# Performance work log

Measured on AMD Instinct MI355X. Metric: run time of the kernel, lower is better.

Reference implementation:

```python
import jax, jax.numpy as jnp
import numpy as np

PATCH = 9
RAD = PATCH // 2  # 4


def _spatial_correlation(a, b):
    """SpatialCorrelationSampler(kernel_size=1, patch_size=9, stride=1,
    padding=0, dilation_patch=1).
    a, b: [B, C, H, W] -> out: [B, 9, 9, H, W]
    out[b, pi, pj, i, j] = sum_c a[b,c,i,j] * b_zeropad[b,c, i+pi-4, j+pj-4]
    Computed one shift at a time (81 small reductions) so we never
    materialize an 81x-unfolded copy of b.
    """
    B, C, H, W = a.shape
    bp = jnp.pad(b, ((0, 0), (0, 0), (RAD, RAD), (RAD, RAD)))
    rows = []
    for di in range(PATCH):
        cols = []
        for dj in range(PATCH):
            # shifted view of b, then channel-dot with a -> [B, H, W]
            cols.append(jnp.sum(a * bp[:, :, di:di + H, dj:dj + W], axis=1))
        rows.append(jnp.stack(cols, axis=1))  # [B, 9, H, W]
    return jnp.stack(rows, axis=1)  # [B, 9, 9, H, W]


def setup_inputs() -> dict:
    key = jax.random.key(0)
    shapes = [(8, 64, 112, 112), (8, 128, 56, 56), (8, 256, 28, 28), (8, 512, 14, 14)]
    keys = jax.random.split(key, 8)
    inp = {}
    for i, s in enumerate(shapes):
        inp[f"rgb{i}"] = jax.random.normal(keys[i], s, dtype=jnp.float32)
        inp[f"depth{i}"] = jax.random.normal(keys[4 + i], s, dtype=jnp.float32)
    return inp


def reference(rgb0, rgb1, rgb2, rgb3, depth0, depth1, depth2, depth3):
    rgbs = [rgb0, rgb1, rgb2, rgb3]
    depths = [depth0, depth1, depth2, depth3]
    corrs = []
    for i in range(4):
        corrs.insert(0, _spatial_correlation(rgbs[i], depths[i]))
    # reversed order: (corr3, corr2, corr1, corr0)
    return tuple(corrs)
```

## Files before the change

kernel.cpp:

```cpp
#include <hip/hip_runtime.h>

#define THREADS 256

#define OFF3 0
#define OFF2 127008
#define OFF1 635040
#define OFF0 2667168

#define N1 2032128
#define N2 508032
#define N3 127008
#define WS_L1 0
#define WS_L2 (2 * N1)
#define WS_L3 (WS_L2 + 4 * N2)
#define WS_FLOATS (WS_L3 + 16 * N3)
#define WS_BYTES ((size_t)WS_FLOATS * 4)

#define GB_L0 448
#define GB_L1 224
#define GB_L2 224
#define GB_L3 512
#define GB_TOT (GB_L0 + GB_L1 + GB_L2 + GB_L3)

#define SMEM_FLOATS 8320

__global__ void __launch_bounds__(THREADS)
zero_region_kernel(float* __restrict__ p, int n) {
    int i = blockIdx.x * blockDim.x + threadIdx.x;
    int stride = gridDim.x * blockDim.x;
    for (; i < n; i += stride) p[i] = 0.f;
}

__device__ __forceinline__ void gload16(const float* g, float* l) {
    __builtin_amdgcn_global_load_lds(
        (const __attribute__((address_space(1))) void*)g,
        (__attribute__((address_space(3))) void*)l, 16, 0, 0);
}
__device__ __forceinline__ void gload4(const float* g, float* l) {
    __builtin_amdgcn_global_load_lds(
        (const __attribute__((address_space(1))) void*)g,
        (__attribute__((address_space(3))) void*)l, 4, 0, 0);
}

template<int C, int H, int W, int TI, int TW, int SJ, int STRIPS, int CHUNKS,
         int CB, int MODE>
__device__ __forceinline__ void corr_level(const float* __restrict__ a,
                                           const float* __restrict__ b,
                                           float* __restrict__ out,
                                           int blk, float* __restrict__ smem)
{
    constexpr int PER_I = 9 * STRIPS;
    constexpr int USED  = TI * PER_I;
    constexpr bool F4   = (W % 4 == 0) && (TW % 4 == 0) && (SJ % 4 == 0);
    constexpr int BWQ0  = (TW + 8 + 3) / 4 + 1;
    constexpr int BWQ   = (BWQ0 % 2 == 0) ? BWQ0 + 1 : BWQ0;
    constexpr int BW_   = F4 ? BWQ * 4
                             : (((TW + 8 + 1) / 2) * 2);
    constexpr bool F2   = !F4 && (SJ % 2 == 0) && (TW % 2 == 0);
    constexpr int BROWS = TI + 8;
    constexpr int CCH   = C / CHUNKS;
    constexpr int HT    = (H + TI - 1) / TI;
    constexpr int WT    = W / TW;
    constexpr int NOUT  = 8 * 81 * H * W;
    constexpr int HW    = H * W;
    constexpr int BPC   = BROWS * BW_;
    constexpr int APC   = TI * TW;
    constexpr int BUFSZ = CB * (BPC + APC);
    constexpr int A_OFF = CB * BPC;
    constexpr int NG    = CCH / CB;
    static_assert(USED <= THREADS, "thread mapping overflow");
    static_assert(SJ * STRIPS == TW, "strips must cover TW");
    static_assert(CCH % CB == 0, "CB must divide channels per chunk");
    static_assert(2 * BUFSZ <= SMEM_FLOATS, "smem overflow");
    static_assert(BUFSZ % 4 == 0 && A_OFF % 4 == 0 && APC % 2 == 0, "alignment");

    const int ch = blk % CHUNKS;
    int t = blk / CHUNKS;
    const int jt = t % WT; t /= WT;
    const int it = t % HT;
    const int bb = t / HT;
    const int i0 = it * TI;
    const int jb = jt * TW;

    const int tid = threadIdx.x;
    const int ii  = tid / PER_I;
    const int rem = tid - ii * PER_I;
    const int pi  = rem / STRIPS;
    const int s   = rem - pi * STRIPS;
    const int j0  = s * SJ;
    const bool active = (tid < USED) &&
                        ((H % TI == 0) || (i0 + ii) < H);

    const int c0 = ch * CCH;
    const float* __restrict__ bp = b + (size_t)(bb * C + c0) * HW;
    const float* __restrict__ ap = a + (size_t)(bb * C + c0) * HW;

    float acc[9][SJ];
    #pragma unroll
    for (int p = 0; p < 9; ++p)
        #pragma unroll
        for (int u = 0; u < SJ; ++u) acc[p][u] = 0.f;

    constexpr int F4PR = BW_ / 4;
    constexpr int NBF4 = BROWS * F4PR;
    constexpr int TOT4 = CB * NBF4;
    constexpr int K4   = (TOT4 + THREADS - 1) / THREADS;
    constexpr int TOTS = CB * BPC;
    constexpr int KS   = (TOTS + THREADS - 1) / THREADS;
    constexpr int A4PR = TW / 4;
    constexpr int NAF4 = TI * A4PR;
    constexpr int ATOT4 = CB * NAF4;
    constexpr int KA4  = (ATOT4 + THREADS - 1) / THREADS;
    constexpr int ATOTS = CB * APC;
    constexpr int KAS  = (ATOTS + THREADS - 1) / THREADS;

    const int wbase = tid & ~63;

    auto stage = [&](int cg, float* buf) {
        const float* gb = bp + (size_t)(cg * CB) * HW;
        const float* ga = ap + (size_t)(cg * CB) * HW;
        if constexpr (F4) {
            #pragma unroll
            for (int k = 0; k < K4; ++k) {
                const int f = tid + k * THREADS;
                const int cb  = f / NBF4;
                const int f2  = f - cb * NBF4;
                const int row = f2 / F4PR;
                const int c4  = f2 - row * F4PR;
                const int r   = i0 + row - 4;
                const int jj  = jb + (c4 - 1) * 4;
                if ((f < TOT4) && ((unsigned)r < (unsigned)H)
                    && (jj >= 0) && (jj <= W - 4))
                    gload16(gb + cb * HW + r * W + jj,
                            buf + (size_t)(k * THREADS + wbase) * 4);
            }
            #pragma unroll
            for (int k = 0; k < KA4; ++k) {
                const int f = tid + k * THREADS;
                const int cb  = f / NAF4;
                const int f2  = f - cb * NAF4;
                const int row = f2 / A4PR;
                const int c4  = f2 - row * A4PR;
                if ((f < ATOT4) && ((H % TI == 0) || (i0 + row) < H))
                    gload16(ga + cb * HW + (i0 + row) * W + jb + c4 * 4,
                            buf + A_OFF + (size_t)(k * THREADS + wbase) * 4);
            }
        } else {
            #pragma unroll
            for (int k = 0; k < KS; ++k) {
                const int f = tid + k * THREADS;
                const int cb  = f / BPC;
                const int f2  = f - cb * BPC;
                const int row = f2 / BW_;
                const int col = f2 - row * BW_;
                const int r   = i0 + row - 4;
                const int jj  = jb + col - 4;
                if ((f < TOTS) && ((unsigned)r < (unsigned)H)
                    && ((unsigned)jj < (unsigned)W))
                    gload4(gb + cb * HW + r * W + jj,
                           buf + (k * THREADS + wbase));
            }
            #pragma unroll
            for (int k = 0; k < KAS; ++k) {
                const int f = tid + k * THREADS;
                const int cb  = f / APC;
                const int f2  = f - cb * APC;
                const int row = f2 / TW;
                const int col = f2 - row * TW;
                if ((f < ATOTS) && ((H % TI == 0) || (i0 + row) < H))
                    gload4(ga + cb * HW + (i0 + row) * W + jb + col,
                           buf + A_OFF + (k * THREADS + wbase));
            }
        }
    };
    auto compute = [&](const float* buf) {
        if (!active) return;
        #pragma unroll
        for (int cb = 0; cb < CB; ++cb) {
            float breg[SJ + 8];
            float areg[SJ];
            const float* bbase = &buf[cb * BPC + (ii + pi) * BW_ + j0];
            const float* abase = &buf[A_OFF + cb * APC + ii * TW + j0];
            if constexpr (F4) {
                #pragma unroll
                for (int k = 0; k < (SJ + 8) / 4; ++k) {
                    float4 v = *reinterpret_cast<const float4*>(&bbase[4 * k]);
                    breg[4*k+0] = v.x; breg[4*k+1] = v.y;
                    breg[4*k+2] = v.z; breg[4*k+3] = v.w;
                }
                #pragma unroll
                for (int u = 0; u < SJ / 4; ++u) {
                    float4 v = *reinterpret_cast<const float4*>(&abase[4 * u]);
                    areg[4*u+0] = v.x; areg[4*u+1] = v.y;
                    areg[4*u+2] = v.z; areg[4*u+3] = v.w;
                }
            } else if constexpr (F2) {
                #pragma unroll
                for (int k = 0; k < (SJ + 8) / 2; ++k) {
                    float2 v = *reinterpret_cast<const float2*>(&bbase[2 * k]);
                    breg[2*k+0] = v.x; breg[2*k+1] = v.y;
                }
                #pragma unroll
                for (int u = 0; u < SJ / 2; ++u) {
                    float2 v = *reinterpret_cast<const float2*>(&abase[2 * u]);
                    areg[2*u+0] = v.x; areg[2*u+1] = v.y;
                }
            } else {
                #pragma unroll
                for (int k = 0; k < SJ + 8; ++k) breg[k] = bbase[k];
                #pragma unroll
                for (int u = 0; u < SJ; ++u) areg[u] = abase[u];
            }
            #pragma unroll
            for (int pj = 0; pj < 9; ++pj)
                #pragma unroll
                for (int u = 0; u < SJ; ++u)
                    acc[pj][u] = fmaf(areg[u], breg[u + pj], acc[pj][u]);
        }
    };

    {
        float4 z = {0.f, 0.f, 0.f, 0.f};
        float4* s4 = reinterpret_cast<float4*>(smem);
        for (int f = tid; f < (2 * BUFSZ) / 4; f += THREADS) s4[f] = z;
    }
    __syncthreads();

    float* bufA = smem;
    float* bufB = smem + BUFSZ;
    stage(0, bufA);
    __syncthreads();

    for (int cg = 0; cg < NG; ++cg) {
        if (cg + 1 < NG) stage(cg + 1, bufB);
        __builtin_amdgcn_s_setprio(1);
        compute(bufA);
        __builtin_amdgcn_s_setprio(0);
        __syncthreads();
        float* tp = bufA; bufA = bufB; bufB = tp;
    }

    if (active) {
        const int i = i0 + ii;
        float* obase = out;
        if constexpr (MODE == 1) obase = out + (size_t)ch * NOUT;
        #pragma unroll
        for (int pj = 0; pj < 9; ++pj) {
            float* o = obase + ((size_t)((bb * 9 + pi) * 9 + pj) * H + i) * W + jb + j0;
            if constexpr (MODE == 2) {
                #pragma unroll
                for (int u = 0; u < SJ; ++u) atomicAdd(&o[u], acc[pj][u]);
            } else if constexpr (F4) {
                #pragma unroll
                for (int u = 0; u < SJ / 4; ++u) {
                    float4 v;
                    v.x = acc[pj][4*u+0]; v.y = acc[pj][4*u+1];
                    v.z = acc[pj][4*u+2]; v.w = acc[pj][4*u+3];
                    *reinterpret_cast<float4*>(&o[4 * u]) = v;
                }
            } else {
                #pragma unroll
                for (int u = 0; u < SJ; ++u) o[u] = acc[pj][u];
            }
        }
    }
}

template<int PMODE>
__global__ void __launch_bounds__(THREADS)
corr_fused(const float* __restrict__ a0, const float* __restrict__ b0,
           const float* __restrict__ a1, const float* __restrict__ b1,
           const float* __restrict__ a2, const float* __restrict__ b2,
           const float* __restrict__ a3, const float* __restrict__ b3,
           float* __restrict__ out, float* __restrict__ ws)
{
    __shared__ float smem[SMEM_FLOATS];
    const int blk = blockIdx.x;
    if (blk < GB_L0) {
        corr_level<64, 112, 112, 4, 56, 8, 7, 1, 4, 0>(
            a0, b0, out + OFF0, blk, smem);
    } else if (blk < GB_L0 + GB_L1) {
        corr_level<128, 56, 56, 4, 56, 8, 7, 2, 4, PMODE>(
            a1, b1, PMODE == 1 ? ws + WS_L1 : out + OFF1, blk - GB_L0, smem);
    } else if (blk < GB_L0 + GB_L1 + GB_L2) {
        corr_level<256, 28, 28, 4, 28, 4, 7, 4, 4, PMODE>(
            a2, b2, PMODE == 1 ? ws + WS_L2 : out + OFF2, blk - (GB_L0 + GB_L1), smem);
    } else {
        corr_level<512, 14, 14, 4, 14, 2, 7, 16, 8, PMODE>(
            a3, b3, PMODE == 1 ? ws + WS_L3 : out + OFF3,
            blk - (GB_L0 + GB_L1 + GB_L2), smem);
    }
}

__global__ void __launch_bounds__(THREADS)
reduce_all_kernel(const float* __restrict__ ws, float* __restrict__ out)
{
    const int blk = blockIdx.x;
    const float4* src; float4* dst; int n4, chunks, nb, base;
    if (blk < 96)       { src = (const float4*)(ws + WS_L3); dst = (float4*)(out + OFF3);
                          n4 = N3 / 4; chunks = 16; nb = 96;  base = 0; }
    else if (blk < 224) { src = (const float4*)(ws + WS_L2); dst = (float4*)(out + OFF2);
                          n4 = N2 / 4; chunks = 4;  nb = 128; base = 96; }
    else                { src = (const float4*)(ws + WS_L1); dst = (float4*)(out + OFF1);
                          n4 = N1 / 4; chunks = 2;  nb = 288; base = 224; }
    for (int i = (blk - base) * THREADS + threadIdx.x; i < n4; i += nb * THREADS) {
        float4 sv = src[i];
        for (int k = 1; k < chunks; ++k) {
            float4 tv = src[(size_t)k * n4 + i];
            sv.x += tv.x; sv.y += tv.y; sv.z += tv.z; sv.w += tv.w;
        }
        dst[i] = sv;
    }
}

extern "C" void kernel_launch(void* const* d_in, const int* in_sizes, int n_in,
                              void* d_out, int out_size, void* d_ws, size_t ws_size,
                              hipStream_t stream) {
    const float* a0 = (const float*)d_in[0];
    const float* b0 = (const float*)d_in[1];
    const float* a1 = (const float*)d_in[2];
    const float* b1 = (const float*)d_in[3];
    const float* a2 = (const float*)d_in[4];
    const float* b2 = (const float*)d_in[5];
    const float* a3 = (const float*)d_in[6];
    const float* b3 = (const float*)d_in[7];
    float* out = (float*)d_out;
    float* ws  = (float*)d_ws;

    if (ws_size >= WS_BYTES) {
        hipLaunchKernelGGL((corr_fused<1>), dim3(GB_TOT), dim3(THREADS), 0, stream,
                           a0, b0, a1, b1, a2, b2, a3, b3, out, ws);
        hipLaunchKernelGGL(reduce_all_kernel, dim3(512), dim3(THREADS), 0, stream,
                           ws, out);
    } else {
        hipLaunchKernelGGL(zero_region_kernel, dim3(512), dim3(THREADS), 0, stream,
                           out, OFF0);
        hipLaunchKernelGGL((corr_fused<2>), dim3(GB_TOT), dim3(THREADS), 0, stream,
                           a0, b0, a1, b1, a2, b2, a3, b3, out, ws);
    }
}
```

Measured before the change: 70.39 us.

## Switch to triple-buffered LDS pipeline with explicit vmcnt waits and zero-page loads

Replaces the double-buffered stage/compute loop with a three-buffer pipeline that prefetches two channel groups ahead. Each group waits with explicit s_waitcnt counts and a single barrier instead of two __syncthreads. Out-of-bounds loads now read from a global zero page rather than being skipped, so the upfront LDS zero-fill and its barrier go away. Channel group sizes are halved so three buffers fit in LDS. This trades smaller compute batches per barrier for deeper overlap, and relies on the hand-counted vmcnt values matching the number of loads issued.

```diff
diff --git a/kernel.cpp b/kernel.cpp
--- a/kernel.cpp
+++ b/kernel.cpp
@@ -22,7 +22,9 @@
 #define GB_L3 512
 #define GB_TOT (GB_L0 + GB_L1 + GB_L2 + GB_L3)
 
-#define SMEM_FLOATS 8320
+#define SMEM_FLOATS 9216
+
+__device__ __attribute__((aligned(64))) const float g_zeropage[16] = {};
 
 __global__ void __launch_bounds__(THREADS)
 zero_region_kernel(float* __restrict__ p, int n) {
@@ -40,6 +42,19 @@
     __builtin_amdgcn_global_load_lds(
         (const __attribute__((address_space(1))) void*)g,
         (__attribute__((address_space(3))) void*)l, 4, 0, 0);
+}
+
+template<int N> __device__ __forceinline__ void wait_vm_lgkm0() {
+    static_assert(N >= 0 && N <= 8, "unsupported count");
+    if constexpr (N == 0) asm volatile("s_waitcnt vmcnt(0) lgkmcnt(0)" ::: "memory");
+    else if constexpr (N == 1) asm volatile("s_waitcnt vmcnt(1) lgkmcnt(0)" ::: "memory");
+    else if constexpr (N == 2) asm volatile("s_waitcnt vmcnt(2) lgkmcnt(0)" ::: "memory");
+    else if constexpr (N == 3) asm volatile("s_waitcnt vmcnt(3) lgkmcnt(0)" ::: "memory");
+    else if constexpr (N == 4) asm volatile("s_waitcnt vmcnt(4) lgkmcnt(0)" ::: "memory");
+    else if constexpr (N == 5) asm volatile("s_waitcnt vmcnt(5) lgkmcnt(0)" ::: "memory");
+    else if constexpr (N == 6) asm volatile("s_waitcnt vmcnt(6) lgkmcnt(0)" ::: "memory");
+    else if constexpr (N == 7) asm volatile("s_waitcnt vmcnt(7) lgkmcnt(0)" ::: "memory");
+    else                       asm volatile("s_waitcnt vmcnt(8) lgkmcnt(0)" ::: "memory");
 }
 
 template<int C, int H, int W, int TI, int TW, int SJ, int STRIPS, int CHUNKS,
@@ -65,41 +80,7 @@
     constexpr int HW    = H * W;
     constexpr int BPC   = BROWS * BW_;
     constexpr int APC   = TI * TW;
-    constexpr int BUFSZ = CB * (BPC + APC);
-    constexpr int A_OFF = CB * BPC;
     constexpr int NG    = CCH / CB;
-    static_assert(USED <= THREADS, "thread mapping overflow");
-    static_assert(SJ * STRIPS == TW, "strips must cover TW");
-    static_assert(CCH % CB == 0, "CB must divide channels per chunk");
-    static_assert(2 * BUFSZ <= SMEM_FLOATS, "smem overflow");
-    static_assert(BUFSZ % 4 == 0 && A_OFF % 4 == 0 && APC % 2 == 0, "alignment");
-
-    const int ch = blk % CHUNKS;
-    int t = blk / CHUNKS;
-    const int jt = t % WT; t /= WT;
-    const int it = t % HT;
-    const int bb = t / HT;
-    const int i0 = it * TI;
-    const int jb = jt * TW;
-
-    const int tid = threadIdx.x;
-    const int ii  = tid / PER_I;
-    const int rem = tid - ii * PER_I;
-    const int pi  = rem / STRIPS;
-    const int s   = rem - pi * STRIPS;
-    const int j0  = s * SJ;
-    const bool active = (tid < USED) &&
-                        ((H % TI == 0) || (i0 + ii) < H);
-
-    const int c0 = ch * CCH;
-    const float* __restrict__ bp = b + (size_t)(bb * C + c0) * HW;
-    const float* __restrict__ ap = a + (size_t)(bb * C + c0) * HW;
-
-    float acc[9][SJ];
-    #pragma unroll
-    for (int p = 0; p < 9; ++p)
-        #pragma unroll
-        for (int u = 0; u < SJ; ++u) acc[p][u] = 0.f;
 
     constexpr int F4PR = BW_ / 4;
     constexpr int NBF4 = BROWS * F4PR;
@@ -114,6 +95,45 @@
     constexpr int ATOTS = CB * APC;
     constexpr int KAS  = (ATOTS + THREADS - 1) / THREADS;
 
+    constexpr int A_OFF = F4 ? (K4 * THREADS * 4) : (KS * THREADS);
+    constexpr int BUFSZ = F4 ? ((K4 + KA4) * THREADS * 4)
+                             : ((KS + KAS) * THREADS);
+    constexpr int KTOT  = F4 ? (K4 + KA4) : (KS + KAS);
+
+    static_assert(USED <= THREADS, "thread mapping overflow");
+    static_assert(SJ * STRIPS == TW, "strips must cover TW");
+    static_assert(CCH % CB == 0, "CB must divide channels per chunk");
+    static_assert(NG >= 2, "pipeline needs >=2 groups");
+    static_assert(3 * BUFSZ <= SMEM_FLOATS, "smem overflow");
+
+    const int ch = blk % CHUNKS;
+    int t = blk / CHUNKS;
+    const int jt = t % WT; t /= WT;
+    const int it = t % HT;
+    const int bb = t / HT;
+    const int i0 = it * TI;
+    const int jb = jt * TW;
+
+    const int tid = threadIdx.x;
+    const int ii  = tid / PER_I;
+    const int rem = tid - ii * PER_I;
+    const int pi  = rem / STRIPS;
+    const int s   = rem - pi * STRIPS;
+    const int j0  = s * SJ;
+    const bool active = (tid < USED) &&
+                        ((H % TI == 0) || (i0 + ii) < H);
+
+    const int c0 = ch * CCH;
+    const float* __restrict__ bp = b + (size_t)(bb * C + c0) * HW;
+    const float* __restrict__ ap = a + (size_t)(bb * C + c0) * HW;
+    const float* zp = g_zeropage;
+
+    float acc[9][SJ];
+    #pragma unroll
+    for (int p = 0; p < 9; ++p)
+        #pragma unroll
+        for (int u = 0; u < SJ; ++u) acc[p][u] = 0.f;
+
     const int wbase = tid & ~63;
 
     auto stage = [&](int cg, float* buf) {
@@ -129,10 +149,10 @@
                 const int c4  = f2 - row * F4PR;
                 const int r   = i0 + row - 4;
                 const int jj  = jb + (c4 - 1) * 4;
-                if ((f < TOT4) && ((unsigned)r < (unsigned)H)
-                    && (jj >= 0) && (jj <= W - 4))
-                    gload16(gb + cb * HW + r * W + jj,
-                            buf + (size_t)(k * THREADS + wbase) * 4);
+                const bool ok = (f < TOT4) && ((unsigned)r < (unsigned)H)
+                                && (jj >= 0) && (jj <= W - 4);
+                const float* src = ok ? (gb + cb * HW + r * W + jj) : zp;
+                gload16(src, buf + (size_t)(k * THREADS + wbase) * 4);
             }
             #pragma unroll
             for (int k = 0; k < KA4; ++k) {
@@ -141,9 +161,10 @@
                 const int f2  = f - cb * NAF4;
                 const int row = f2 / A4PR;
                 const int c4  = f2 - row * A4PR;
-                if ((f < ATOT4) && ((H % TI == 0) || (i0 + row) < H))
-                    gload16(ga + cb * HW + (i0 + row) * W + jb + c4 * 4,
-                            buf + A_OFF + (size_t)(k * THREADS + wbase) * 4);
+                const bool ok = (f < ATOT4) && ((H % TI == 0) || (i0 + row) < H);
+                const float* src = ok ? (ga + cb * HW + (i0 + row) * W + jb + c4 * 4)
+                                      : zp;
+                gload16(src, buf + A_OFF + (size_t)(k * THREADS + wbase) * 4);
             }
         } else {
             #pragma unroll
@@ -155,10 +176,10 @@
                 const int col = f2 - row * BW_;
                 const int r   = i0 + row - 4;
                 const int jj  = jb + col - 4;
-                if ((f < TOTS) && ((unsigned)r < (unsigned)H)
-                    && ((unsigned)jj < (unsigned)W))
-                    gload4(gb + cb * HW + r * W + jj,
-                           buf + (k * THREADS + wbase));
+                const bool ok = (f < TOTS) && ((unsigned)r < (unsigned)H)
+                                && ((unsigned)jj < (unsigned)W);
+                const float* src = ok ? (gb + cb * HW + r * W + jj) : zp;
+                gload4(src, buf + (k * THREADS + wbase));
             }
             #pragma unroll
             for (int k = 0; k < KAS; ++k) {
@@ -167,9 +188,10 @@
                 const int f2  = f - cb * APC;
                 const int row = f2 / TW;
                 const int col = f2 - row * TW;
-                if ((f < ATOTS) && ((H % TI == 0) || (i0 + row) < H))
-                    gload4(ga + cb * HW + (i0 + row) * W + jb + col,
-                           buf + A_OFF + (k * THREADS + wbase));
+                const bool ok = (f < ATOTS) && ((H % TI == 0) || (i0 + row) < H);
+                const float* src = ok ? (ga + cb * HW + (i0 + row) * W + jb + col)
+                                      : zp;
+                gload4(src, buf + A_OFF + (k * THREADS + wbase));
             }
         }
     };
@@ -219,25 +241,20 @@
         }
     };
 
-    {
-        float4 z = {0.f, 0.f, 0.f, 0.f};
-        float4* s4 = reinterpret_cast<float4*>(smem);
-        for (int f = tid; f < (2 * BUFSZ) / 4; f += THREADS) s4[f] = z;
-    }
-    __syncthreads();
-
     float* bufA = smem;
     float* bufB = smem + BUFSZ;
+    float* bufC = smem + 2 * BUFSZ;
+
     stage(0, bufA);
-    __syncthreads();
-
+    stage(1, bufB);
     for (int cg = 0; cg < NG; ++cg) {
-        if (cg + 1 < NG) stage(cg + 1, bufB);
-        __builtin_amdgcn_s_setprio(1);
+        if (cg < NG - 1) wait_vm_lgkm0<KTOT>();
+        else             wait_vm_lgkm0<0>();
+        __builtin_amdgcn_s_barrier();
+        __builtin_amdgcn_sched_barrier(0);
+        if (cg + 2 < NG) stage(cg + 2, bufC);
         compute(bufA);
-        __builtin_amdgcn_s_setprio(0);
-        __syncthreads();
-        float* tp = bufA; bufA = bufB; bufB = tp;
+        float* tp = bufA; bufA = bufB; bufB = bufC; bufC = tp;
     }
 
     if (active) {
@@ -277,16 +294,16 @@
     __shared__ float smem[SMEM_FLOATS];
     const int blk = blockIdx.x;
     if (blk < GB_L0) {
-        corr_level<64, 112, 112, 4, 56, 8, 7, 1, 4, 0>(
+        corr_level<64, 112, 112, 4, 56, 8, 7, 1, 2, 0>(
             a0, b0, out + OFF0, blk, smem);
     } else if (blk < GB_L0 + GB_L1) {
-        corr_level<128, 56, 56, 4, 56, 8, 7, 2, 4, PMODE>(
+        corr_level<128, 56, 56, 4, 56, 8, 7, 2, 2, PMODE>(
             a1, b1, PMODE == 1 ? ws + WS_L1 : out + OFF1, blk - GB_L0, smem);
     } else if (blk < GB_L0 + GB_L1 + GB_L2) {
-        corr_level<256, 28, 28, 4, 28, 4, 7, 4, 4, PMODE>(
+        corr_level<256, 28, 28, 4, 28, 4, 7, 4, 2, PMODE>(
             a2, b2, PMODE == 1 ? ws + WS_L2 : out + OFF2, blk - (GB_L0 + GB_L1), smem);
     } else {
-        corr_level<512, 14, 14, 4, 14, 2, 7, 16, 8, PMODE>(
+        corr_level<512, 14, 14, 4, 14, 2, 7, 16, 4, PMODE>(
             a3, b3, PMODE == 1 ? ws + WS_L3 : out + OFF3,
             blk - (GB_L0 + GB_L1 + GB_L2), smem);
     }
```

Measured after the change: 67.55 us. 4.0% less time.
